# Performance work log

Measured on AMD Instinct MI355X. Metric: run time of the kernel, lower is better.

## Reference

```python
import jax, jax.numpy as jnp
import numpy as np

B, D, NB, BS = 32, 2048, 16, 512  # batch, dim_input=dim_output, n_blocks, block_size; NB*BS*BS == D*D


def setup_inputs() -> dict:
    key = jax.random.key(0)
    k1, k2, k3, k4, k5 = jax.random.split(key, 5)
    x = jax.random.normal(k1, (B, D), dtype=jnp.float32)
    gate_w = jax.random.normal(k2, (D, NB), dtype=jnp.float32) / np.sqrt(D)
    gate_b = jax.random.normal(k3, (NB,), dtype=jnp.float32) * 0.02
    weight = jax.random.normal(k4, (D, D), dtype=jnp.float32) / np.sqrt(D)  # kaiming-uniform-like scale
    bias = jax.random.normal(k5, (D,), dtype=jnp.float32) * (1.0 / np.sqrt(D))
    return {"x": x, "gate_w": gate_w, "gate_b": gate_b, "weight": weight, "bias": bias}


def reference(x, gate_w, gate_b, weight, bias):
    b = x.shape[0]
    k_drop = NB // 2
    # gate network: Linear -> Sigmoid
    g = jax.nn.sigmoid(x @ gate_w + gate_b)  # (b, NB)
    # zero out the k smallest gates per sample (topk largest=False, scatter 0)
    _, drop_idx = jax.lax.top_k(-g, k_drop)  # indices of smallest gates
    rows = jnp.arange(b)[:, None]
    g = g.at[rows, drop_idx].set(0.0)
    # broadcast gates over block-diagonal chunks of weight
    w0 = weight.reshape(NB, BS, BS)
    gw = (g[:, :, None, None] * w0).reshape(b, D, D)  # (b, dim_output, dim_input)
    # batched matvec + bias
    return jnp.einsum('bij,bj->bi', gw, x) + bias
```

## Files before the change

### kernel.cpp

```cpp
#include <hip/hip_runtime.h>
#include <hip/hip_bf16.h>


#define D_DIM 2048
#define B_DIM 32
#define NB_DIM 16
#define NWAVE 8
#define KCHUNK (D_DIM / NWAVE)

typedef __attribute__((ext_vector_type(4))) float f32x4;
typedef __attribute__((ext_vector_type(8))) float f32x8;
typedef __attribute__((ext_vector_type(8))) __bf16 bf16x8;

static __device__ __forceinline__ __bf16 f2bf(float f) {
    unsigned u = __builtin_bit_cast(unsigned, f);
    u += 0x7fffu + ((u >> 16) & 1u);
    unsigned short h = (unsigned short)(u >> 16);
    return __builtin_bit_cast(__bf16, h);
}

static __device__ __forceinline__ bf16x8 load_cvt8(const float* p) {
    const f32x8 v = *(const f32x8*)p;
    bf16x8 r;
#pragma unroll
    for (int i = 0; i < 8; ++i) r[i] = f2bf(v[i]);
    return r;
}

__global__ __launch_bounds__(256) void gate_part(
    const float* __restrict__ X,
    const float* __restrict__ GW,
    float* __restrict__ gp)
{
    __shared__ float red[NB_DIM][256];
    const int b  = blockIdx.x >> 3;
    const int ks = blockIdx.x & 7;
    const int t  = threadIdx.x;
    const int c  = ks * 256 + t;

    const float xv = X[b * D_DIM + c];
    const f32x4 g0 = *(const f32x4*)(GW + c * NB_DIM + 0);
    const f32x4 g1 = *(const f32x4*)(GW + c * NB_DIM + 4);
    const f32x4 g2 = *(const f32x4*)(GW + c * NB_DIM + 8);
    const f32x4 g3 = *(const f32x4*)(GW + c * NB_DIM + 12);

#pragma unroll
    for (int n = 0; n < 4; ++n) red[n][t]      = xv * g0[n];
#pragma unroll
    for (int n = 0; n < 4; ++n) red[n + 4][t]  = xv * g1[n];
#pragma unroll
    for (int n = 0; n < 4; ++n) red[n + 8][t]  = xv * g2[n];
#pragma unroll
    for (int n = 0; n < 4; ++n) red[n + 12][t] = xv * g3[n];
    __syncthreads();

    for (int s = 128; s > 0; s >>= 1) {
        if (t < s) {
#pragma unroll
            for (int n = 0; n < NB_DIM; ++n) red[n][t] += red[n][t + s];
        }
        __syncthreads();
    }
    if (t < NB_DIM) gp[b * (8 * NB_DIM) + ks * NB_DIM + t] = red[t][0];
}

__global__ __launch_bounds__(512) void mega(
    const float* __restrict__ W,
    const float* __restrict__ X,
    const float* __restrict__ gp,
    const float* __restrict__ GB,
    const float* __restrict__ bias,
    float* __restrict__ out)
{
    __shared__ float pm[NWAVE][16][20];
    __shared__ float sg[16];

    const int bid  = blockIdx.x;
    const int rt   = bid & 127;
    const int bh   = bid >> 7;
    const int wave = threadIdx.x >> 6;
    const int lane = threadIdx.x & 63;
    const int l15  = lane & 15;
    const int q    = lane >> 4;

    const int r0 = rt * 16;
    const int k0 = wave * KCHUNK;

    const float* arow = W + (size_t)(r0 + l15) * D_DIM + k0 + q * 8;
    const float* xrow = X + (size_t)(bh * 16 + l15) * D_DIM + k0 + q * 8;

    f32x4 acc = {0.f, 0.f, 0.f, 0.f};
#pragma unroll
    for (int kk = 0; kk < KCHUNK / 32; ++kk) {
        const bf16x8 av = load_cvt8(arow + kk * 32);
        const bf16x8 bv = load_cvt8(xrow + kk * 32);
        acc = __builtin_amdgcn_mfma_f32_16x16x32_bf16(av, bv, acc, 0, 0, 0);
    }
    *(f32x4*)&pm[wave][l15][q * 4] = acc;

    if (threadIdx.x < NB_DIM) {
        const int b = bh * 16 + threadIdx.x;
        const float* p = gp + b * (8 * NB_DIM);
        float lg[NB_DIM];
#pragma unroll
        for (int n = 0; n < NB_DIM; ++n) lg[n] = GB[n];
#pragma unroll
        for (int ks = 0; ks < 8; ++ks)
#pragma unroll
            for (int n = 0; n < NB_DIM; ++n) lg[n] += p[ks * NB_DIM + n];
        float g[NB_DIM];
#pragma unroll
        for (int n = 0; n < NB_DIM; ++n) g[n] = 1.f / (1.f + __expf(-lg[n]));
        const int nb = rt >> 3;
        float gn = 0.f;
#pragma unroll
        for (int n = 0; n < NB_DIM; ++n) gn = (n == nb) ? g[n] : gn;
        int rank = 0;
#pragma unroll
        for (int m = 0; m < NB_DIM; ++m)
            if (g[m] < gn || (g[m] == gn && m < nb)) rank++;
        sg[threadIdx.x] = (rank >= NB_DIM / 2) ? gn : 0.f;
    }
    __syncthreads();

    if (threadIdx.x < 64) {
        const int lb = threadIdx.x >> 2;
        const int r4 = (threadIdx.x & 3) * 4;
        f32x4 s = {0.f, 0.f, 0.f, 0.f};
#pragma unroll
        for (int w = 0; w < NWAVE; ++w)
            s += *(const f32x4*)&pm[w][lb][r4];
        const float gv = sg[lb];
        const f32x4 bi = *(const f32x4*)(bias + r0 + r4);
        f32x4 y;
#pragma unroll
        for (int i = 0; i < 4; ++i) y[i] = gv * s[i] + bi[i];
        *(f32x4*)(out + (size_t)(bh * 16 + lb) * D_DIM + r0 + r4) = y;
    }
}

extern "C" void kernel_launch(void* const* d_in, const int* in_sizes, int n_in,
                              void* d_out, int out_size, void* d_ws, size_t ws_size,
                              hipStream_t stream) {
    const float* x    = (const float*)d_in[0];
    const float* gw   = (const float*)d_in[1];
    const float* gb   = (const float*)d_in[2];
    const float* w    = (const float*)d_in[3];
    const float* bias = (const float*)d_in[4];
    float* out = (float*)d_out;

    float* gp = (float*)d_ws;

    gate_part<<<B_DIM * 8, 256, 0, stream>>>(x, gw, gp);
    mega<<<256, 512, 0, stream>>>(w, x, gp, gb, bias, out);
}
```

Baseline: 83.05 us.

## Fuse gate projection into main kernel using split-bf16 MFMA

Removes the separate gate_part kernel launch and its workspace round-trip. Each block now recomputes the 16x16 gate logits for its batch half with extra MFMAs on bf16 hi/lo splits of x and gate weights, which keeps near-fp32 accuracy for the top-k selection. The trade-off is redundant gate computation in all 128 row-tile blocks, three extra MFMAs and strided gate-weight loads per iteration, and more shared memory and barriers.

```diff
diff --git a/kernel.cpp b/kernel.cpp
--- a/kernel.cpp
+++ b/kernel.cpp
@@ -19,6 +19,11 @@
     return __builtin_bit_cast(__bf16, h);
 }
 
+static __device__ __forceinline__ float bf2f(__bf16 h) {
+    unsigned u = ((unsigned)__builtin_bit_cast(unsigned short, h)) << 16;
+    return __builtin_bit_cast(float, u);
+}
+
 static __device__ __forceinline__ bf16x8 load_cvt8(const float* p) {
     const f32x8 v = *(const f32x8*)p;
     bf16x8 r;
@@ -27,52 +32,17 @@
     return r;
 }
 
-__global__ __launch_bounds__(256) void gate_part(
-    const float* __restrict__ X,
-    const float* __restrict__ GW,
-    float* __restrict__ gp)
-{
-    __shared__ float red[NB_DIM][256];
-    const int b  = blockIdx.x >> 3;
-    const int ks = blockIdx.x & 7;
-    const int t  = threadIdx.x;
-    const int c  = ks * 256 + t;
-
-    const float xv = X[b * D_DIM + c];
-    const f32x4 g0 = *(const f32x4*)(GW + c * NB_DIM + 0);
-    const f32x4 g1 = *(const f32x4*)(GW + c * NB_DIM + 4);
-    const f32x4 g2 = *(const f32x4*)(GW + c * NB_DIM + 8);
-    const f32x4 g3 = *(const f32x4*)(GW + c * NB_DIM + 12);
-
-#pragma unroll
-    for (int n = 0; n < 4; ++n) red[n][t]      = xv * g0[n];
-#pragma unroll
-    for (int n = 0; n < 4; ++n) red[n + 4][t]  = xv * g1[n];
-#pragma unroll
-    for (int n = 0; n < 4; ++n) red[n + 8][t]  = xv * g2[n];
-#pragma unroll
-    for (int n = 0; n < 4; ++n) red[n + 12][t] = xv * g3[n];
-    __syncthreads();
-
-    for (int s = 128; s > 0; s >>= 1) {
-        if (t < s) {
-#pragma unroll
-            for (int n = 0; n < NB_DIM; ++n) red[n][t] += red[n][t + s];
-        }
-        __syncthreads();
-    }
-    if (t < NB_DIM) gp[b * (8 * NB_DIM) + ks * NB_DIM + t] = red[t][0];
-}
-
 __global__ __launch_bounds__(512) void mega(
     const float* __restrict__ W,
     const float* __restrict__ X,
-    const float* __restrict__ gp,
+    const float* __restrict__ GW,
     const float* __restrict__ GB,
     const float* __restrict__ bias,
     float* __restrict__ out)
 {
-    __shared__ float pm[NWAVE][16][20];
+    __shared__ float pm [NWAVE][16][20];
+    __shared__ float pmg[NWAVE][16][20];
+    __shared__ float sgm[16][17];
     __shared__ float sg[16];
 
     const int bid  = blockIdx.x;
@@ -86,40 +56,63 @@
     const int r0 = rt * 16;
     const int k0 = wave * KCHUNK;
 
-    const float* arow = W + (size_t)(r0 + l15) * D_DIM + k0 + q * 8;
-    const float* xrow = X + (size_t)(bh * 16 + l15) * D_DIM + k0 + q * 8;
+    const float* arow = W  + (size_t)(r0 + l15) * D_DIM + k0 + q * 8;
+    const float* xrow = X  + (size_t)(bh * 16 + l15) * D_DIM + k0 + q * 8;
+    const float* gwp  = GW + (size_t)(k0 + q * 8) * NB_DIM + l15;
 
-    f32x4 acc = {0.f, 0.f, 0.f, 0.f};
+    f32x4 acc  = {0.f, 0.f, 0.f, 0.f};
+    f32x4 gacc = {0.f, 0.f, 0.f, 0.f};
+
 #pragma unroll
     for (int kk = 0; kk < KCHUNK / 32; ++kk) {
         const bf16x8 av = load_cvt8(arow + kk * 32);
-        const bf16x8 bv = load_cvt8(xrow + kk * 32);
-        acc = __builtin_amdgcn_mfma_f32_16x16x32_bf16(av, bv, acc, 0, 0, 0);
+
+        const f32x8 xv = *(const f32x8*)(xrow + kk * 32);
+        bf16x8 bhi, blo;
+#pragma unroll
+        for (int i = 0; i < 8; ++i) {
+            bhi[i] = f2bf(xv[i]);
+            blo[i] = f2bf(xv[i] - bf2f(bhi[i]));
+        }
+        bf16x8 ghi, glo;
+#pragma unroll
+        for (int j = 0; j < 8; ++j) {
+            const float gv = gwp[(kk * 32 + j) * NB_DIM];
+            ghi[j] = f2bf(gv);
+            glo[j] = f2bf(gv - bf2f(ghi[j]));
+        }
+
+        acc  = __builtin_amdgcn_mfma_f32_16x16x32_bf16(av,  bhi, acc,  0, 0, 0);
+        gacc = __builtin_amdgcn_mfma_f32_16x16x32_bf16(ghi, bhi, gacc, 0, 0, 0);
+        gacc = __builtin_amdgcn_mfma_f32_16x16x32_bf16(ghi, blo, gacc, 0, 0, 0);
+        gacc = __builtin_amdgcn_mfma_f32_16x16x32_bf16(glo, bhi, gacc, 0, 0, 0);
     }
-    *(f32x4*)&pm[wave][l15][q * 4] = acc;
 
-    if (threadIdx.x < NB_DIM) {
-        const int b = bh * 16 + threadIdx.x;
-        const float* p = gp + b * (8 * NB_DIM);
-        float lg[NB_DIM];
+    *(f32x4*)&pm [wave][l15][q * 4] = acc;
+    *(f32x4*)&pmg[wave][l15][q * 4] = gacc;
+    __syncthreads();
+
+    if (threadIdx.x < 256) {
+        const int lb = threadIdx.x >> 4;
+        const int n  = threadIdx.x & 15;
+        float s = GB[n];
 #pragma unroll
-        for (int n = 0; n < NB_DIM; ++n) lg[n] = GB[n];
-#pragma unroll
-        for (int ks = 0; ks < 8; ++ks)
-#pragma unroll
-            for (int n = 0; n < NB_DIM; ++n) lg[n] += p[ks * NB_DIM + n];
-        float g[NB_DIM];
-#pragma unroll
-        for (int n = 0; n < NB_DIM; ++n) g[n] = 1.f / (1.f + __expf(-lg[n]));
+        for (int w = 0; w < NWAVE; ++w) s += pmg[w][lb][n];
+        sgm[lb][n] = 1.f / (1.f + __expf(-s));
+    }
+    __syncthreads();
+
+    if (threadIdx.x < 16) {
+        const int lb = threadIdx.x;
         const int nb = rt >> 3;
-        float gn = 0.f;
-#pragma unroll
-        for (int n = 0; n < NB_DIM; ++n) gn = (n == nb) ? g[n] : gn;
+        const float gn = sgm[lb][nb];
         int rank = 0;
 #pragma unroll
-        for (int m = 0; m < NB_DIM; ++m)
-            if (g[m] < gn || (g[m] == gn && m < nb)) rank++;
-        sg[threadIdx.x] = (rank >= NB_DIM / 2) ? gn : 0.f;
+        for (int m = 0; m < NB_DIM; ++m) {
+            const float gm = sgm[lb][m];
+            if (gm < gn || (gm == gn && m < nb)) rank++;
+        }
+        sg[lb] = (rank >= NB_DIM / 2) ? gn : 0.f;
     }
     __syncthreads();
 
@@ -149,8 +142,5 @@
     const float* bias = (const float*)d_in[4];
     float* out = (float*)d_out;
 
-    float* gp = (float*)d_ws;
-
-    gate_part<<<B_DIM * 8, 256, 0, stream>>>(x, gw, gp);
-    mega<<<256, 512, 0, stream>>>(w, x, gp, gb, bias, out);
+    mega<<<256, 512, 0, stream>>>(w, x, gw, gb, bias, out);
 }
```

Result: faster. 80.95 us (-2.5%).
